# Performance work log

Hardware: AMD Instinct MI355X
Metric: run time of the kernel (lower is better)

The kernel has to match this reference:

```python
import jax, jax.numpy as jnp
import numpy as np

N_NODES = 100000
N_EDGES = 1600000
IN_F = 128
HID = 16
NEG_SLOPE = 0.2


def setup_inputs() -> dict:
    key = jax.random.key(0)
    ks = jax.random.split(key, 12)
    x = jax.random.normal(ks[0], (N_NODES, IN_F), dtype=jnp.float32)
    edge_index = jax.random.randint(ks[1], (2, N_EDGES), 0, N_NODES, dtype=jnp.int32)
    s1 = 1.0 / np.sqrt(IN_F)
    s2 = 1.0 / np.sqrt(2 * HID)
    # layer 1: heads=2, out=16, concat -> 32
    W1 = jax.random.normal(ks[2], (IN_F, 2 * HID), dtype=jnp.float32) * s1
    a_src1 = jax.random.normal(ks[3], (2, HID), dtype=jnp.float32) * s2
    a_dst1 = jax.random.normal(ks[4], (2, HID), dtype=jnp.float32) * s2
    b1 = jnp.zeros((2 * HID,), dtype=jnp.float32)
    # layer 2: heads=1, out=1
    W2 = jax.random.normal(ks[5], (2 * HID, 1), dtype=jnp.float32) * s2
    a_src2 = jax.random.normal(ks[6], (1, 1), dtype=jnp.float32)
    a_dst2 = jax.random.normal(ks[7], (1, 1), dtype=jnp.float32)
    b2 = jnp.zeros((1,), dtype=jnp.float32)
    return {"x": x, "edge_index": edge_index, "W1": W1, "a_src1": a_src1,
            "a_dst1": a_dst1, "b1": b1, "W2": W2, "a_src2": a_src2,
            "a_dst2": a_dst2, "b2": b2}


def gat_conv(x, src, dst, W, a_src, a_dst, bias, heads, out_ch, concat):
    # PyG GATConv: linear proj, per-edge leaky-relu score, segment softmax over
    # incoming edges (dst), scatter-add aggregation. Self loops already in src/dst.
    n = x.shape[0]
    h = (x @ W).reshape(n, heads, out_ch)                      # [N,H,C]
    alpha_s = (h * a_src[None]).sum(-1)                        # [N,H]
    alpha_d = (h * a_dst[None]).sum(-1)                        # [N,H]
    e = jax.nn.leaky_relu(alpha_s[src] + alpha_d[dst], NEG_SLOPE)  # [E,H]
    m = jax.lax.stop_gradient(jax.ops.segment_max(e, dst, num_segments=n))
    ex = jnp.exp(e - m[dst])
    denom = jax.ops.segment_sum(ex, dst, num_segments=n)       # [N,H]
    alpha = ex / (denom[dst] + 1e-16)                          # [E,H]
    out = jax.ops.segment_sum(alpha[..., None] * h[src], dst, num_segments=n)  # [N,H,C]
    out = out.reshape(n, heads * out_ch) if concat else out.mean(axis=1)
    return out + bias


def reference(x, edge_index, W1, a_src1, a_dst1, b1, W2, a_src2, a_dst2, b2):
    n = x.shape[0]
    loop = jnp.arange(n, dtype=edge_index.dtype)
    src = jnp.concatenate([edge_index[0], loop])
    dst = jnp.concatenate([edge_index[1], loop])
    h = jax.nn.elu(gat_conv(x, src, dst, W1, a_src1, a_dst1, b1, 2, HID, True))
    out = gat_conv(h, src, dst, W2, a_src2, a_dst2, b2, 1, 1, False)
    return out
```

## Files before the change

### kernel.cpp

```cpp
#include <hip/hip_runtime.h>
#include <math.h>

#define IN_F 128
#define C1 32
#define NEG 0.2f
#define BSZ 128
#define CAP 2560
#define EPB 2048
#define TPW 2
#define KBE 5

typedef _Float16 h16;
typedef _Float16 h16x2 __attribute__((ext_vector_type(2)));
typedef _Float16 h16x4 __attribute__((ext_vector_type(4)));
typedef _Float16 h16x8 __attribute__((ext_vector_type(8)));
typedef float f32x4 __attribute__((ext_vector_type(4)));

__device__ __forceinline__ float leaky(float x) { return x >= 0.f ? x : NEG * x; }

__global__ __launch_bounds__(256)
void k_fat(const float* __restrict__ x, const float* __restrict__ W1,
           const float* __restrict__ a_s, const float* __restrict__ a_d,
           h16* __restrict__ h1h, float* __restrict__ as1,
           float* __restrict__ ad1, int N,
           const int* __restrict__ ei, int E, int ET, int nbk,
           int* __restrict__ bcnt, int* __restrict__ ebuf, int nproj) {
    __shared__ int smem[6144];
    int t = threadIdx.x;
    if ((int)blockIdx.x < nproj) {
        int wid = t >> 6, lane = t & 63;
        int q = lane >> 4, r = lane & 15;
        h16x8 Bf[2][4];
        #pragma unroll
        for (int ct = 0; ct < 2; ++ct)
            #pragma unroll
            for (int kc = 0; kc < 4; ++kc)
                #pragma unroll
                for (int j = 0; j < 8; ++j)
                    Bf[ct][kc][j] = (h16)W1[(kc * 32 + q * 8 + j) * C1 + ct * 16 + r];
        float a_s0 = a_s[r], a_s1v = a_s[16 + r];
        float a_d0 = a_d[r], a_d1v = a_d[16 + r];
        #pragma unroll
        for (int tt = 0; tt < TPW; ++tt) {
            int tile = (blockIdx.x * 4 + wid) * TPW + tt;
            int m0 = tile << 4;
            if (m0 >= N) break;
            int row = m0 + r; if (row >= N) row = N - 1;
            const float* xr = x + (size_t)row * IN_F + q * 8;
            f32x4 acc0 = {0.f, 0.f, 0.f, 0.f};
            f32x4 acc1 = {0.f, 0.f, 0.f, 0.f};
            #pragma unroll
            for (int kc = 0; kc < 4; ++kc) {
                float4 xa = *(const float4*)(xr + kc * 32);
                float4 xb = *(const float4*)(xr + kc * 32 + 4);
                h16x8 A;
                A[0] = (h16)xa.x; A[1] = (h16)xa.y; A[2] = (h16)xa.z; A[3] = (h16)xa.w;
                A[4] = (h16)xb.x; A[5] = (h16)xb.y; A[6] = (h16)xb.z; A[7] = (h16)xb.w;
                acc0 = __builtin_amdgcn_mfma_f32_16x16x32_f16(A, Bf[0][kc], acc0, 0, 0, 0);
                acc1 = __builtin_amdgcn_mfma_f32_16x16x32_f16(A, Bf[1][kc], acc1, 0, 0, 0);
            }
            #pragma unroll
            for (int reg = 0; reg < 4; ++reg) {
                int node = m0 + q * 4 + reg;
                bool vld = node < N;
                float h0 = acc0[reg], h1 = acc1[reg];
                if (vld) {
                    h1h[(size_t)node * C1 + r]      = (h16)h0;
                    h1h[(size_t)node * C1 + 16 + r] = (h16)h1;
                }
                float s0 = h0 * a_s0, s1 = h1 * a_s1v;
                float d0 = h0 * a_d0, d1 = h1 * a_d1v;
                s0 += __shfl_xor(s0, 1); s0 += __shfl_xor(s0, 2); s0 += __shfl_xor(s0, 4); s0 += __shfl_xor(s0, 8);
                s1 += __shfl_xor(s1, 1); s1 += __shfl_xor(s1, 2); s1 += __shfl_xor(s1, 4); s1 += __shfl_xor(s1, 8);
                d0 += __shfl_xor(d0, 1); d0 += __shfl_xor(d0, 2); d0 += __shfl_xor(d0, 4); d0 += __shfl_xor(d0, 8);
                d1 += __shfl_xor(d1, 1); d1 += __shfl_xor(d1, 2); d1 += __shfl_xor(d1, 4); d1 += __shfl_xor(d1, 8);
                if (vld && r == 0) {
                    *(float2*)&as1[node * 2] = make_float2(s0, s1);
                    *(float2*)&ad1[node * 2] = make_float2(d0, d1);
                }
            }
        }
    } else {
        int* hist = smem;
        int* lcur = hist + 1024;
        int2* ecache = (int2*)(lcur + 1024);
        int bid = blockIdx.x - nproj;
        hist[t] = 0; hist[t + 256] = 0; hist[t + 512] = 0; hist[t + 768] = 0;
        __syncthreads();
        int i0 = bid * EPB, i1 = min(ET, i0 + EPB);
        for (int i = i0 + t; i < i1; i += 256) {
            int s, d;
            if (i < E) { s = ei[i]; d = ei[E + i]; } else { s = d = i - E; }
            ecache[i - i0] = make_int2(s, d);
            atomicAdd(&hist[d >> 7], 1);
        }
        __syncthreads();
        for (int b = t; b < nbk; b += 256) {
            int h = hist[b];
            int base = h ? atomicAdd(&bcnt[b], h) : 0;
            lcur[b] = b * CAP + base;
        }
        __syncthreads();
        for (int i = i0 + t; i < i1; i += 256) {
            int2 e = ecache[i - i0];
            int bkt = e.y >> 7;
            int pos = atomicAdd(&lcur[bkt], 1);
            if (pos < (bkt + 1) * CAP)
                ebuf[pos] = (e.x << 7) | (e.y & 127);
        }
    }
}

__global__ __launch_bounds__(512)
void k_bagg(const int* __restrict__ bcnt, const int* __restrict__ ebuf,
            int N,
            const float* __restrict__ as1, const float* __restrict__ ad1,
            const float* __restrict__ b1, const float* __restrict__ W2,
            const h16* __restrict__ h1h, float* __restrict__ p2) {
    __shared__ int2 elist[CAP];
    __shared__ int deg[BSZ], sst[BSZ], cur[BSZ];
    __shared__ float adl[BSZ * 2];
    __shared__ float b1s[C1], w2s[C1];
    int b = blockIdx.x, t = threadIdx.x;
    int n0 = b * BSZ;
    int cnt = min(bcnt[b], CAP);
    int ebase = b * CAP;
    if (t < BSZ) {
        deg[t] = 0;
        int n = n0 + t;
        float2 v = (n < N) ? ((const float2*)ad1)[n] : make_float2(0.f, 0.f);
        adl[t * 2] = v.x; adl[t * 2 + 1] = v.y;
    }
    if (t >= 128 && t < 128 + C1) { b1s[t - 128] = b1[t - 128]; w2s[t - 128] = W2[t - 128]; }
    __syncthreads();
    int rec[KBE], wp[KBE];
    #pragma unroll
    for (int k = 0; k < KBE; ++k) {
        int i = t + k * 512;
        if (i < cnt) {
            int e = ebuf[ebase + i];
            int dl = e & 127, s = e >> 7;
            rec[k] = e;
            atomicAdd(&deg[dl], 1);
            float2 asv = ((const float2*)as1)[s];
            float w0 = __expf(leaky(asv.x + adl[dl * 2 + 0]));
            float w1 = __expf(leaky(asv.y + adl[dl * 2 + 1]));
            h16x2 wv = { (h16)w0, (h16)w1 };
            wp[k] = *(int*)&wv;
        } else rec[k] = -1;
    }
    __syncthreads();
    int v = (t < BSZ) ? deg[t] : 0;
    __syncthreads();
    for (int o = 1; o < BSZ; o <<= 1) {
        int xv = (t >= o && t < BSZ) ? deg[t - o] : 0;
        __syncthreads();
        if (t < BSZ) deg[t] += xv;
        __syncthreads();
    }
    if (t < BSZ) {
        int excl = deg[t] - v;
        sst[t] = excl; cur[t] = excl;
    }
    __syncthreads();
    #pragma unroll
    for (int k = 0; k < KBE; ++k) {
        if (rec[k] >= 0) {
            int dl = rec[k] & 127;
            int p = atomicAdd(&cur[dl], 1);
            int2 r2; r2.x = rec[k] >> 7; r2.y = wp[k];
            elist[p] = r2;
        }
    }
    __syncthreads();
    int l = t & 3, slot = t >> 2, c0 = l * 8, head = l >> 1;
    int node = n0 + slot;
    if (node >= N) return;
    int j0 = sst[slot], j1 = deg[slot];
    float den = 0.f;
    float acc[8] = {0.f, 0.f, 0.f, 0.f, 0.f, 0.f, 0.f, 0.f};
    for (int j = j0; j < j1; j += 8) {
        #pragma unroll
        for (int k = 0; k < 8; ++k) {
            int jj = j + k;
            bool valid = jj < j1;
            jj = valid ? jj : j0;
            int2 e = elist[jj];
            int s = e.x;
            h16x2 wv = *(h16x2*)&e.y;
            float w = valid ? (float)(head ? wv.y : wv.x) : 0.f;
            h16x8 hv = *(const h16x8*)(h1h + ((size_t)s << 5) + c0);
            den += w;
            #pragma unroll
            for (int i2 = 0; i2 < 8; ++i2)
                acc[i2] = fmaf(w, (float)hv[i2], acc[i2]);
        }
    }
    float inv = 1.f / (den + 1e-16f);
    float val = 0.f;
    #pragma unroll
    for (int i2 = 0; i2 < 8; ++i2) {
        float o = acc[i2] * inv + b1s[c0 + i2];
        o = o > 0.f ? o : expm1f(o);
        val = fmaf(o, w2s[c0 + i2], val);
    }
    val += __shfl_xor(val, 1); val += __shfl_xor(val, 2);
    if (l == 0) p2[node] = val;
}

__global__ __launch_bounds__(512)
void k_l2(const int* __restrict__ bcnt, const int* __restrict__ ebuf,
          const float* __restrict__ p2, const float* __restrict__ as2,
          const float* __restrict__ ad2, const float* __restrict__ b2,
          float* __restrict__ out, int N) {
    __shared__ float den[BSZ], num[BSZ], pdl[BSZ];
    int b = blockIdx.x, t = threadIdx.x;
    int n0 = b * BSZ;
    if (t < BSZ) {
        den[t] = 0.f; num[t] = 0.f;
        int n = n0 + t;
        pdl[t] = (n < N) ? ad2[0] * p2[n] : 0.f;
    }
    __syncthreads();
    float A = as2[0];
    int cnt = min(bcnt[b], CAP);
    int ebase = b * CAP;
    for (int i = t; i < cnt; i += 512) {
        int e = ebuf[ebase + i];
        int dl = e & 127, s = e >> 7;
        float ps = p2[s];
        float w = __expf(leaky(fmaf(ps, A, pdl[dl])));
        atomicAdd(&den[dl], w);
        atomicAdd(&num[dl], w * ps);
    }
    __syncthreads();
    if (t < BSZ && n0 + t < N)
        out[n0 + t] = num[t] / (den[t] + 1e-16f) + b2[0];
}

extern "C" void kernel_launch(void* const* d_in, const int* in_sizes, int n_in,
                              void* d_out, int out_size, void* d_ws, size_t ws_size,
                              hipStream_t stream) {
    const float* x    = (const float*)d_in[0];
    const int*   ei   = (const int*)d_in[1];
    const float* W1   = (const float*)d_in[2];
    const float* a_s1 = (const float*)d_in[3];
    const float* a_d1 = (const float*)d_in[4];
    const float* b1   = (const float*)d_in[5];
    const float* W2   = (const float*)d_in[6];
    const float* a_s2 = (const float*)d_in[7];
    const float* a_d2 = (const float*)d_in[8];
    const float* b2   = (const float*)d_in[9];
    float* out = (float*)d_out;

    const int N  = in_sizes[0] / IN_F;
    const int E  = in_sizes[1] / 2;
    const int ET = E + N;
    const int nbk = (N + BSZ - 1) / BSZ;

    float* w   = (float*)d_ws;
    float* as1 = w; w += (size_t)2 * N;
    float* ad1 = w; w += (size_t)2 * N;
    float* p2  = w; w += (size_t)N;
    h16* h1h   = (h16*)w;
    w += (size_t)16 * N;
    int* iw     = (int*)w;
    int* bcnt   = iw; iw += 1024;
    int* ebuf   = iw; iw += (size_t)nbk * CAP;

    const int B = 256;
    const int ntile = (N + 15) / 16;
    const int nproj = (ntile + 4 * TPW - 1) / (4 * TPW);
    const int nblkA = (ET + EPB - 1) / EPB;

    hipMemsetAsync(bcnt, 0, 1024 * sizeof(int), stream);
    k_fat <<<nproj + nblkA, B, 0, stream>>>(x, W1, a_s1, a_d1, h1h, as1, ad1, N,
                                            ei, E, ET, nbk, bcnt, ebuf, nproj);
    k_bagg<<<nbk, 512, 0, stream>>>(bcnt, ebuf, N, as1, ad1, b1, W2, h1h, p2);
    k_l2  <<<nbk, 512, 0, stream>>>(bcnt, ebuf, p2, a_s2, a_d2, b2, out, N);
}
```

Before: 187.3 us.

## Keep edge records in registers and interleave projection and scatter blocks

The scatter path now holds each thread's 8 edges (packed record plus bucket id) in registers instead of an int2 LDS cache, shrinking the fused kernel's shared memory from 24KB to 8KB. Block indices are also remapped so projection and edge-bucketing blocks alternate across the grid rather than running as two separate phases. The goals are higher occupancy and running the compute-bound MFMA projection alongside the memory- and atomic-bound scatter. The cost is more registers in the scatter branch and a fixed KME=8 loop that assumes EPB equals 8×256.

```diff
diff --git a/kernel.cpp b/kernel.cpp
--- a/kernel.cpp
+++ b/kernel.cpp
@@ -8,6 +8,7 @@
 #define CAP 2560
 #define EPB 2048
 #define TPW 2
+#define KME 8
 #define KBE 5
 
 typedef _Float16 h16;
@@ -25,9 +26,16 @@
            float* __restrict__ ad1, int N,
            const int* __restrict__ ei, int E, int ET, int nbk,
            int* __restrict__ bcnt, int* __restrict__ ebuf, int nproj) {
-    __shared__ int smem[6144];
+    __shared__ int smem[2048];
     int t = threadIdx.x;
-    if ((int)blockIdx.x < nproj) {
+    int bid = blockIdx.x;
+    int nmsc = (int)gridDim.x - nproj;
+    int m = min(nproj, nmsc);
+    bool isProj; int id;
+    if (bid < 2 * m) { isProj = !(bid & 1); id = bid >> 1; }
+    else if (nproj > m) { isProj = true;  id = bid - m; }
+    else               { isProj = false; id = bid - nproj; }
+    if (isProj) {
         int wid = t >> 6, lane = t & 63;
         int q = lane >> 4, r = lane & 15;
         h16x8 Bf[2][4];
@@ -42,7 +50,7 @@
         float a_d0 = a_d[r], a_d1v = a_d[16 + r];
         #pragma unroll
         for (int tt = 0; tt < TPW; ++tt) {
-            int tile = (blockIdx.x * 4 + wid) * TPW + tt;
+            int tile = (id * 4 + wid) * TPW + tt;
             int m0 = tile << 4;
             if (m0 >= N) break;
             int row = m0 + r; if (row >= N) row = N - 1;
@@ -83,16 +91,20 @@
     } else {
         int* hist = smem;
         int* lcur = hist + 1024;
-        int2* ecache = (int2*)(lcur + 1024);
-        int bid = blockIdx.x - nproj;
         hist[t] = 0; hist[t + 256] = 0; hist[t + 512] = 0; hist[t + 768] = 0;
         __syncthreads();
-        int i0 = bid * EPB, i1 = min(ET, i0 + EPB);
-        for (int i = i0 + t; i < i1; i += 256) {
-            int s, d;
-            if (i < E) { s = ei[i]; d = ei[E + i]; } else { s = d = i - E; }
-            ecache[i - i0] = make_int2(s, d);
-            atomicAdd(&hist[d >> 7], 1);
+        int i0 = id * EPB, i1 = min(ET, i0 + EPB);
+        int rec[KME], bk[KME];
+        #pragma unroll
+        for (int k = 0; k < KME; ++k) {
+            int i = i0 + k * 256 + t;
+            if (i < i1) {
+                int s, d;
+                if (i < E) { s = ei[i]; d = ei[E + i]; } else { s = d = i - E; }
+                rec[k] = (s << 7) | (d & 127);
+                bk[k] = d >> 7;
+                atomicAdd(&hist[bk[k]], 1);
+            } else bk[k] = -1;
         }
         __syncthreads();
         for (int b = t; b < nbk; b += 256) {
@@ -101,12 +113,13 @@
             lcur[b] = b * CAP + base;
         }
         __syncthreads();
-        for (int i = i0 + t; i < i1; i += 256) {
-            int2 e = ecache[i - i0];
-            int bkt = e.y >> 7;
-            int pos = atomicAdd(&lcur[bkt], 1);
-            if (pos < (bkt + 1) * CAP)
-                ebuf[pos] = (e.x << 7) | (e.y & 127);
+        #pragma unroll
+        for (int k = 0; k < KME; ++k) {
+            if (bk[k] >= 0) {
+                int pos = atomicAdd(&lcur[bk[k]], 1);
+                if (pos < (bk[k] + 1) * CAP)
+                    ebuf[pos] = rec[k];
+            }
         }
     }
 }
```

New measurement: 193.7 us. +3.4%, slower.
